# Kernel tuning notes

Measured on AMD Instinct MI355X. Metric: run time of the kernel, lower is better.

The kernel has to match this reference:

```python
import jax, jax.numpy as jnp
import numpy as np

INPUT_DIM = 784
HIDDEN = 4096
BATCH = 64
T = 30                      # time_steps
TAU = 100.0                 # tau_mem
DECAY = 1.0 - 1.0 / TAU     # LIF leak per step
THR = 0.5                   # spike threshold
SCALE = 16.0                # input_scale
K = int(HIDDEN * 0.08)      # k-WTA k = hidden_dim * sparsity = 327


def setup_inputs() -> dict:
    key = jax.random.key(0)
    k1, k2, k3 = jax.random.split(key, 3)
    x = jax.random.uniform(k1, (BATCH, INPUT_DIM), dtype=jnp.float32)
    W1 = jax.random.normal(k2, (INPUT_DIM, HIDDEN), dtype=jnp.float32) * 0.05
    W2 = jax.random.normal(k3, (HIDDEN, HIDDEN), dtype=jnp.float32) * 0.02
    return {"x": x, "W1": W1, "W2": W2}


def _kwta(s):
    # k-WTA: keep units >= k-th largest value per row (binary spikes -> this
    # matches torch.topk kth-value thresholding; if row sum==0 it's a no-op).
    vals = jax.lax.top_k(s, K)[0]           # [B, K]
    thresh = vals[:, -1:]                   # [B, 1]
    return s * (s >= thresh).astype(s.dtype)


def _lif(v, cur):
    # Leaky integrate-and-fire: decay, integrate, hard-threshold, reset-to-zero.
    v = v * DECAY + cur
    s = (v >= THR).astype(v.dtype)
    return v * (1.0 - s), s


def reference(x, W1, W2):
    # prepare_input: normalize by max and scale (x.max()>0 branch)
    x = x / jnp.maximum(jnp.max(x), jnp.float32(1e-12)) * SCALE
    B = x.shape[0]

    def step(carry, _):
        v0, v1, v2, sum0, sum1, sum2 = carry
        v0, s0 = _lif(v0, x)                # Retina: external current each step
        v1, s1 = _lif(v1, s0 @ W1)          # V1 feedforward
        v2, s2 = _lif(v2, s1 @ W2)          # V2 feedforward
        s1m = _kwta(s1)                     # k-WTA applied to returned spikes
        s2m = _kwta(s2)
        return (v0, v1, v2, sum0 + s0, sum1 + s1m, sum2 + s2m), None

    z0 = jnp.zeros((B, INPUT_DIM), jnp.float32)
    zh = jnp.zeros((B, HIDDEN), jnp.float32)
    carry = (z0, zh, zh, z0, zh, zh)
    (_, _, _, sum0, sum1, sum2), _ = jax.lax.scan(step, carry, None, length=T)
    # mean firing rates per group (spike_sums / time_steps)
    return (sum0 / T, sum1 / T, sum2 / T)
```

## Files before the change

kernel.cpp:

```cpp
#include <hip/hip_runtime.h>
#include <cstdint>
#include <cstddef>

#define INPUT_DIM 784
#define HIDDEN    4096
#define BATCH     64
#define T_STEPS   30
#define N0 (BATCH*INPUT_DIM)
#define N1 (BATCH*HIDDEN)
#define M_ROWS (T_STEPS*BATCH)
#define NDIG 4
#define MB_CNT (M_ROWS/32)
#define KC1 25
#define KC2 128

typedef int v4i  __attribute__((ext_vector_type(4)));
typedef int v16i __attribute__((ext_vector_type(16)));

__global__ __launch_bounds__(256) void max_kernel(const float* __restrict__ x,
                                                  unsigned* __restrict__ maxbits) {
    int i = blockIdx.x * 256 + threadIdx.x;
    float v = (i < N0) ? x[i] : 0.0f;
    #pragma unroll
    for (int off = 32; off > 0; off >>= 1)
        v = fmaxf(v, __shfl_down(v, off, 64));
    __shared__ float sm[4];
    int lane = threadIdx.x & 63;
    int wv   = threadIdx.x >> 6;
    if (lane == 0) sm[wv] = v;
    __syncthreads();
    if (threadIdx.x == 0) {
        float m = fmaxf(fmaxf(sm[0], sm[1]), fmaxf(sm[2], sm[3]));
        atomicMax(maxbits, __float_as_uint(m));
    }
}

__global__ __launch_bounds__(256) void lif0_kernel(const float* __restrict__ x,
                                                   const unsigned* __restrict__ maxbits,
                                                   uint8_t* __restrict__ AF1,
                                                   float* __restrict__ out0) {
    int j = blockIdx.x * 256 + threadIdx.x;
    int b = blockIdx.y;
    if (j >= INPUT_DIM) return;
    float mx = fmaxf(__uint_as_float(*maxbits), 1e-12f);
    float xs = __fmul_rn(__fdiv_rn(x[b * INPUT_DIM + j], mx), 16.0f);
    int kc = j >> 5;
    int lane = (b & 31) | (((j >> 4) & 1) << 5);
    size_t base = (((size_t)(kc * MB_CNT + (b >> 5)) * 64 + lane) << 4) + (j & 15);
    float v = 0.0f;
    int cnt = 0;
    #pragma unroll
    for (int t = 0; t < T_STEPS; ++t) {
        v = __fadd_rn(__fmul_rn(v, 0.99f), xs);
        int s = (v >= 0.5f) ? 1 : 0;
        cnt += s;
        v = s ? 0.0f : v;
        AF1[base + (size_t)t * 2048] = (uint8_t)s;
    }
    out0[b * INPUT_DIM + j] = (float)cnt / 30.0f;
}

__global__ __launch_bounds__(256) void digitize_kernel(const float* __restrict__ W,
                                                       int8_t* __restrict__ BF,
                                                       int Krows, int KC, double scale) {
    __shared__ float tile[32][33];
    const int nb = blockIdx.x, kc = blockIdx.y;
    const int tid = threadIdx.x;
    {
        int r  = tid >> 3;
        int c4 = (tid & 7) << 2;
        int k  = kc * 32 + r;
        float4 w4 = make_float4(0.f, 0.f, 0.f, 0.f);
        if (k < Krows)
            w4 = *(const float4*)&W[(size_t)k * HIDDEN + nb * 32 + c4];
        tile[r][c4]     = w4.x;
        tile[r][c4 + 1] = w4.y;
        tile[r][c4 + 2] = w4.z;
        tile[r][c4 + 3] = w4.w;
    }
    __syncthreads();
    const int d    = tid >> 6;
    const int lane = tid & 63;
    const int nl   = lane & 31;
    const int kh   = (lane >> 5) << 4;
    char dig[16];
    #pragma unroll
    for (int jj = 0; jj < 16; ++jj) {
        double w = (double)tile[kh + jj][nl];
        long long q = __double2ll_rn(w * scale);
        int dd = 0;
        #pragma unroll
        for (int dd_i = 0; dd_i <= 3; ++dd_i) {
            dd = (int)(((q + 128) & 255) - 128);
            q = (q - (long long)dd) >> 8;
            if (dd_i == d) break;
        }
        dig[jj] = (char)dd;
    }
    *(int4*)&BF[((((size_t)nb * KC + kc) * NDIG + d) << 10) + (lane << 4)] =
        *(int4*)&dig[0];
}

#define MFMA_GRP(A0, A1, B0, B1, B2, B3)                                        \
    acc[0][0] = __builtin_amdgcn_mfma_i32_32x32x32_i8(A0, B0, acc[0][0], 0, 0, 0); \
    acc[1][0] = __builtin_amdgcn_mfma_i32_32x32x32_i8(A1, B0, acc[1][0], 0, 0, 0); \
    acc[0][1] = __builtin_amdgcn_mfma_i32_32x32x32_i8(A0, B1, acc[0][1], 0, 0, 0); \
    acc[1][1] = __builtin_amdgcn_mfma_i32_32x32x32_i8(A1, B1, acc[1][1], 0, 0, 0); \
    acc[0][2] = __builtin_amdgcn_mfma_i32_32x32x32_i8(A0, B2, acc[0][2], 0, 0, 0); \
    acc[1][2] = __builtin_amdgcn_mfma_i32_32x32x32_i8(A1, B2, acc[1][2], 0, 0, 0); \
    acc[0][3] = __builtin_amdgcn_mfma_i32_32x32x32_i8(A0, B3, acc[0][3], 0, 0, 0); \
    acc[1][3] = __builtin_amdgcn_mfma_i32_32x32x32_i8(A1, B3, acc[1][3], 0, 0, 0)

__device__ __forceinline__ void gload16(const int8_t* g, int8_t* l) {
    __builtin_amdgcn_global_load_lds(
        (const __attribute__((address_space(1))) void*)g,
        (__attribute__((address_space(3))) void*)l, 16, 0, 0);
}

#define STAGE(BUF, KCV)                                                          \
    do {                                                                         \
        gload16(gA  + (size_t)(KCV) * astride, &lds[BUF][       (wave << 10)]);  \
        gload16(gB0 + (size_t)(KCV) * bstride, &lds[BUF][4096 + (wave << 10)]);  \
        gload16(gB1 + (size_t)(KCV) * bstride, &lds[BUF][8192 + (wave << 10)]);  \
    } while (0)

#define ITER(S, WN, DOSTAGE, KCV)                                                \
    do {                                                                         \
        __builtin_amdgcn_sched_barrier(0);                                       \
        asm volatile("s_waitcnt vmcnt(" #WN ")\n\ts_barrier" ::: "memory");      \
        __builtin_amdgcn_sched_barrier(0);                                       \
        v4i a0 = *(const v4i*)&lds[S][ msb      * 1024 + (lane << 4)];           \
        v4i a1 = *(const v4i*)&lds[S][(msb + 1) * 1024 + (lane << 4)];           \
        v4i b0 = *(const v4i*)&lds[S][4096 + ((wave & 1) << 12) +        (lane << 4)]; \
        v4i b1 = *(const v4i*)&lds[S][4096 + ((wave & 1) << 12) + 1024 + (lane << 4)]; \
        v4i b2 = *(const v4i*)&lds[S][4096 + ((wave & 1) << 12) + 2048 + (lane << 4)]; \
        v4i b3 = *(const v4i*)&lds[S][4096 + ((wave & 1) << 12) + 3072 + (lane << 4)]; \
        if (DOSTAGE) { STAGE((S + 3) & 3, (KCV) + 3); }                          \
        MFMA_GRP(a0, a1, b0, b1, b2, b3);                                        \
    } while (0)

template <int KC>
__global__ __launch_bounds__(256, 2) void gemm_i8_kernel(const int8_t* __restrict__ AF,
                                                         const int8_t* __restrict__ BF,
                                                         double* __restrict__ C,
                                                         double scale) {
    __shared__ int8_t lds[4][12288];
    const int tid  = threadIdx.x;
    const int wave = tid >> 6, lane = tid & 63;
    const int i  = blockIdx.x;
    const int p  = (i >= 480) ? 1 : 0;
    const int j  = i - p * 480;
    const int bx = j >> 5;
    const int by = p * 32 + ((j & 7) << 2) + ((j >> 3) & 3);
    const int nb0 = by * 2;
    const int msb = (wave >> 1) * 2;

    const int astride = MB_CNT * 1024;
    const int bstride = NDIG * 1024;
    const int8_t* gA  = AF + (((size_t)(bx * 4) * 64) << 4) + tid * 16;
    const int8_t* gB0 = BF + (((size_t)nb0 * KC * NDIG) << 10) + tid * 16;
    const int8_t* gB1 = gB0 + ((size_t)KC * NDIG << 10);

    v16i acc[2][4] = {};

    STAGE(0, 0);
    STAGE(1, 1);
    STAGE(2, 2);

    constexpr int KCM = ((KC - 4) / 4) * 4;
    for (int kc = 0; kc < KCM; kc += 4) {
        ITER(0, 6, 1, kc);
        ITER(1, 6, 1, kc + 1);
        ITER(2, 6, 1, kc + 2);
        ITER(3, 6, 1, kc + 3);
    }
    if constexpr ((KC & 3) == 0) {
        ITER(0, 6, 1, KCM);
        ITER(1, 6, 0, KCM + 1);
        ITER(2, 3, 0, KCM + 2);
        ITER(3, 0, 0, KCM + 3);
    } else {
        ITER(0, 6, 1, KCM);
        ITER(1, 6, 1, KCM + 1);
        ITER(2, 6, 0, KCM + 2);
        ITER(3, 3, 0, KCM + 3);
        ITER(0, 0, 0, KCM + 4);
    }

    const int col = lane & 31;
    const int rb  = (lane >> 5) << 2;
    const int n_g = by * 64 + (wave & 1) * 32 + col;
    #pragma unroll
    for (int s = 0; s < 2; ++s) {
        const int m_base = bx * 128 + (msb + s) * 32;
        #pragma unroll
        for (int r = 0; r < 16; ++r) {
            int row = (r & 3) + 8 * (r >> 2) + rb;
            long long v = 0;
            #pragma unroll
            for (int d = 3; d >= 0; --d) v = (v << 8) + (long long)acc[s][d][r];
            C[(size_t)(m_base + row) * HIDDEN + n_g] = (double)v * scale;
        }
    }
}

__global__ __launch_bounds__(256) void lif1_kernel(const double* __restrict__ CUR,
                                                   uint8_t* __restrict__ AF,
                                                   float* __restrict__ out1) {
    int e = blockIdx.x * 256 + threadIdx.x;
    int b = e >> 12;
    int j = e & 4095;
    int kc = j >> 5;
    int lane = (b & 31) | (((j >> 4) & 1) << 5);
    size_t base = (((size_t)(kc * MB_CNT + (b >> 5)) * 64 + lane) << 4) + (j & 15);
    double v = 0.0;
    int cnt = 0;
    #pragma unroll
    for (int t = 0; t < T_STEPS; ++t) {
        double cur = CUR[(size_t)t * N1 + e];
        v = __dadd_rn(__dmul_rn(v, 0.99), cur);
        int s = (v >= 0.5) ? 1 : 0;
        cnt += s;
        v = s ? 0.0 : v;
        AF[base + (size_t)t * 2048] = (uint8_t)s;
    }
    out1[e] = (float)cnt / 30.0f;
}

__global__ __launch_bounds__(256) void lif2_kernel(const double* __restrict__ CUR,
                                                   float* __restrict__ out2) {
    int e = blockIdx.x * 256 + threadIdx.x;
    double v = 0.0;
    int cnt = 0;
    #pragma unroll
    for (int t = 0; t < T_STEPS; ++t) {
        double cur = CUR[(size_t)t * N1 + e];
        v = __dadd_rn(__dmul_rn(v, 0.99), cur);
        int s = (v >= 0.5) ? 1 : 0;
        cnt += s;
        v = s ? 0.0 : v;
    }
    out2[e] = (float)cnt / 30.0f;
}

extern "C" void kernel_launch(void* const* d_in, const int* in_sizes, int n_in,
                              void* d_out, int out_size, void* d_ws, size_t ws_size,
                              hipStream_t stream) {
    const float* x  = (const float*)d_in[0];
    const float* W1 = (const float*)d_in[1];
    const float* W2 = (const float*)d_in[2];
    float* out = (float*)d_out;
    char*  ws  = (char*)d_ws;

    const size_t AF1_SZ = (size_t)KC1 * MB_CNT * 1024;
    const size_t BF1_SZ = (size_t)128 * KC1 * NDIG * 1024;
    const size_t AF2_SZ = (size_t)KC2 * MB_CNT * 1024;
    const size_t BF2_SZ = (size_t)128 * KC2 * NDIG * 1024;
    unsigned* maxbits = (unsigned*)ws;
    uint8_t*  AF1 = (uint8_t*)(ws + 256);
    int8_t*   BF1 = (int8_t*)(AF1 + AF1_SZ);
    uint8_t*  AF2 = (uint8_t*)(BF1 + BF1_SZ);
    int8_t*   BF2 = (int8_t*)(AF2 + AF2_SZ);
    double*   CURd = (double*)((char*)BF2 + BF2_SZ);

    float* out0 = out;
    float* out1 = out + N0;
    float* out2 = out + N0 + N1;

    hipMemsetAsync(maxbits, 0, 4, stream);
    hipMemsetAsync(AF1, 0, AF1_SZ, stream);
    max_kernel <<<(N0 + 255) / 256, 256, 0, stream>>>(x, maxbits);
    lif0_kernel<<<dim3(4, BATCH), 256, 0, stream>>>(x, maxbits, AF1, out0);
    digitize_kernel<<<dim3(128, KC1), 256, 0, stream>>>(W1, BF1, INPUT_DIM, KC1,
                                                        4294967296.0);
    digitize_kernel<<<dim3(128, KC2), 256, 0, stream>>>(W2, BF2, HIDDEN, KC2,
                                                        8589934592.0);
    gemm_i8_kernel<KC1><<<960, 256, 0, stream>>>((const int8_t*)AF1, BF1, CURd,
                                                 2.3283064365386963e-10);
    lif1_kernel<<<N1 / 256, 256, 0, stream>>>(CURd, AF2, out1);
    gemm_i8_kernel<KC2><<<960, 256, 0, stream>>>((const int8_t*)AF2, BF2, CURd,
                                                 1.1641532182693481e-10);
    lif2_kernel<<<N1 / 256, 256, 0, stream>>>(CURd, out2);
}
```

Baseline: 302.4 us.

## Load A operand fragments directly into registers with double-buffering instead of via LDS

The A tile is no longer staged through LDS with global_load_lds. Each wave now loads its own A fragments straight from global memory into registers, double-buffered one k-chunk ahead. This shrinks LDS per buffer from 12 KB to 8 KB and removes the LDS reads for A. The vmcnt wait counts are re-tuned to match the new mix of loads. In exchange, each A fragment is fetched by two waves instead of once per block, register pressure rises, and global-load latency for A is hidden only one stage ahead.

```diff
diff --git a/kernel.cpp b/kernel.cpp
--- a/kernel.cpp
+++ b/kernel.cpp
@@ -119,24 +119,26 @@
 
 #define STAGE(BUF, KCV)                                                          \
     do {                                                                         \
-        gload16(gA  + (size_t)(KCV) * astride, &lds[BUF][       (wave << 10)]);  \
-        gload16(gB0 + (size_t)(KCV) * bstride, &lds[BUF][4096 + (wave << 10)]);  \
-        gload16(gB1 + (size_t)(KCV) * bstride, &lds[BUF][8192 + (wave << 10)]);  \
+        gload16(gB0 + (size_t)(KCV) * bstride, &lds[BUF][       (wave << 10)]);  \
+        gload16(gB1 + (size_t)(KCV) * bstride, &lds[BUF][4096 + (wave << 10)]);  \
     } while (0)
 
-#define ITER(S, WN, DOSTAGE, KCV)                                                \
+#define ITER(S, WN, DOSTAGE, DOA, KCV, AC0, AC1, AN0, AN1)                      \
     do {                                                                         \
         __builtin_amdgcn_sched_barrier(0);                                       \
         asm volatile("s_waitcnt vmcnt(" #WN ")\n\ts_barrier" ::: "memory");      \
         __builtin_amdgcn_sched_barrier(0);                                       \
-        v4i a0 = *(const v4i*)&lds[S][ msb      * 1024 + (lane << 4)];           \
-        v4i a1 = *(const v4i*)&lds[S][(msb + 1) * 1024 + (lane << 4)];           \
-        v4i b0 = *(const v4i*)&lds[S][4096 + ((wave & 1) << 12) +        (lane << 4)]; \
-        v4i b1 = *(const v4i*)&lds[S][4096 + ((wave & 1) << 12) + 1024 + (lane << 4)]; \
-        v4i b2 = *(const v4i*)&lds[S][4096 + ((wave & 1) << 12) + 2048 + (lane << 4)]; \
-        v4i b3 = *(const v4i*)&lds[S][4096 + ((wave & 1) << 12) + 3072 + (lane << 4)]; \
+        v4i b0 = *(const v4i*)&lds[S][((wave & 1) << 12) +        (lane << 4)];  \
+        v4i b1 = *(const v4i*)&lds[S][((wave & 1) << 12) + 1024 + (lane << 4)];  \
+        v4i b2 = *(const v4i*)&lds[S][((wave & 1) << 12) + 2048 + (lane << 4)];  \
+        v4i b3 = *(const v4i*)&lds[S][((wave & 1) << 12) + 3072 + (lane << 4)];  \
+        if (DOA) {                                                               \
+            AN0 = *(const v4i*)ap; AN1 = *(const v4i*)(ap + 1024);               \
+            ap += astride;                                                       \
+        }                                                                        \
+        __builtin_amdgcn_sched_barrier(0);                                       \
         if (DOSTAGE) { STAGE((S + 3) & 3, (KCV) + 3); }                          \
-        MFMA_GRP(a0, a1, b0, b1, b2, b3);                                        \
+        MFMA_GRP(AC0, AC1, b0, b1, b2, b3);                                      \
     } while (0)
 
 template <int KC>
@@ -144,7 +146,7 @@
                                                          const int8_t* __restrict__ BF,
                                                          double* __restrict__ C,
                                                          double scale) {
-    __shared__ int8_t lds[4][12288];
+    __shared__ int8_t lds[4][8192];
     const int tid  = threadIdx.x;
     const int wave = tid >> 6, lane = tid & 63;
     const int i  = blockIdx.x;
@@ -154,37 +156,45 @@
     const int by = p * 32 + ((j & 7) << 2) + ((j >> 3) & 3);
     const int nb0 = by * 2;
     const int msb = (wave >> 1) * 2;
+    const int mb0 = bx * 4 + msb;
 
     const int astride = MB_CNT * 1024;
     const int bstride = NDIG * 1024;
-    const int8_t* gA  = AF + (((size_t)(bx * 4) * 64) << 4) + tid * 16;
+    const int8_t* ap = AF + (((size_t)mb0 * 64 + lane) << 4);
     const int8_t* gB0 = BF + (((size_t)nb0 * KC * NDIG) << 10) + tid * 16;
     const int8_t* gB1 = gB0 + ((size_t)KC * NDIG << 10);
 
     v16i acc[2][4] = {};
-
+    v4i ae0, ae1, ao0, ao1;
+
+    ae0 = *(const v4i*)ap; ae1 = *(const v4i*)(ap + 1024); ap += astride;
     STAGE(0, 0);
     STAGE(1, 1);
     STAGE(2, 2);
 
+    ITER(0, 4, 1, 1, 0, ae0, ae1, ao0, ao1);
+    ITER(1, 6, 1, 1, 1, ao0, ao1, ae0, ae1);
+    ITER(2, 6, 1, 1, 2, ae0, ae1, ao0, ao1);
+    ITER(3, 6, 1, 1, 3, ao0, ao1, ae0, ae1);
+
     constexpr int KCM = ((KC - 4) / 4) * 4;
-    for (int kc = 0; kc < KCM; kc += 4) {
-        ITER(0, 6, 1, kc);
-        ITER(1, 6, 1, kc + 1);
-        ITER(2, 6, 1, kc + 2);
-        ITER(3, 6, 1, kc + 3);
+    for (int kc = 4; kc < KCM; kc += 4) {
+        ITER(0, 6, 1, 1, kc,     ae0, ae1, ao0, ao1);
+        ITER(1, 6, 1, 1, kc + 1, ao0, ao1, ae0, ae1);
+        ITER(2, 6, 1, 1, kc + 2, ae0, ae1, ao0, ao1);
+        ITER(3, 6, 1, 1, kc + 3, ao0, ao1, ae0, ae1);
     }
     if constexpr ((KC & 3) == 0) {
-        ITER(0, 6, 1, KCM);
-        ITER(1, 6, 0, KCM + 1);
-        ITER(2, 3, 0, KCM + 2);
-        ITER(3, 0, 0, KCM + 3);
+        ITER(0, 6, 1, 1, KCM,     ae0, ae1, ao0, ao1);
+        ITER(1, 6, 0, 1, KCM + 1, ao0, ao1, ae0, ae1);
+        ITER(2, 4, 0, 1, KCM + 2, ae0, ae1, ao0, ao1);
+        ITER(3, 2, 0, 0, KCM + 3, ao0, ao1, ae0, ae1);
     } else {
-        ITER(0, 6, 1, KCM);
-        ITER(1, 6, 1, KCM + 1);
-        ITER(2, 6, 0, KCM + 2);
-        ITER(3, 3, 0, KCM + 3);
-        ITER(0, 0, 0, KCM + 4);
+        ITER(0, 6, 1, 1, KCM,     ae0, ae1, ao0, ao1);
+        ITER(1, 6, 1, 1, KCM + 1, ao0, ao1, ae0, ae1);
+        ITER(2, 6, 0, 1, KCM + 2, ae0, ae1, ao0, ao1);
+        ITER(3, 4, 0, 1, KCM + 3, ao0, ao1, ae0, ae1);
+        ITER(0, 2, 0, 0, KCM + 4, ae0, ae1, ao0, ao1);
     }
 
     const int col = lane & 31;
```

Measured after the change: 318.4 us. +5.3%, slower.
